# Kernel optimization log

Measured on AMD Instinct MI355X. Metric: run time of the kernel, lower is better.

Reference implementation:

```python
import jax, jax.numpy as jnp
import numpy as np

EPS = 1e-06

def rotate_half(x):
    d = x.shape[-1] // 2
    return jnp.concatenate([-x[..., d:], x[..., :d]], axis=-1)

def rmsnorm(x, w):
    rms = jnp.sqrt(jnp.mean(x * x, axis=-1, keepdims=True) + EPS)
    return (x / rms) * w

def setup_inputs() -> dict:
    key = jax.random.key(0)
    ks = jax.random.split(key, 12)
    H, Hq, Hkv, Dh, S, C = 2048, 16, 8, 128, 1, 16384
    sc = 0.02
    return {
        "hidden_states": jax.random.normal(ks[0], (1, 1, S, H), jnp.float32),
        "cos": jax.random.uniform(ks[1], (1, 1, S, Dh), jnp.float32),
        "sin": jax.random.uniform(ks[2], (1, 1, S, Dh), jnp.float32),
        "attention_mask": jnp.zeros((1, 1, S, C + S), jnp.float32),
        "k_cache": jax.random.normal(ks[3], (Hkv, Dh, C), jnp.float32),
        "v_cache": jax.random.normal(ks[4], (Hkv, C, Dh), jnp.float32),
        "Wq": jax.random.normal(ks[5], (Hq, Dh, H), jnp.float32) * sc,
        "Wk": jax.random.normal(ks[6], (Hkv, Dh, H), jnp.float32) * sc,
        "Wv": jax.random.normal(ks[7], (Hkv, Dh, H), jnp.float32) * sc,
        "Wo": jax.random.normal(ks[8], (H, Hq * Dh), jnp.float32) * sc,
        "q_norm_w": jnp.ones((Dh,), jnp.float32),
        "k_norm_w": jnp.ones((Dh,), jnp.float32),
    }

def reference(hidden_states, cos, sin, attention_mask, k_cache, v_cache, Wq, Wk, Wv, Wo, q_norm_w, k_norm_w):
    S = hidden_states.shape[2]
    Hq, Dh = Wq.shape[0], Wq.shape[1]
    Hkv = Wk.shape[0]
    g = Hq // Hkv
    x = hidden_states.reshape(S, -1)                      # [S, H]
    # per-head 1x1 conv == per-head linear; batched as einsum
    q = rmsnorm(jnp.einsum('sh,qdh->qsd', x, Wq), q_norm_w)   # [Hq, S, Dh]
    k = rmsnorm(jnp.einsum('sh,kdh->ksd', x, Wk), k_norm_w)   # [Hkv, S, Dh]
    v = jnp.einsum('sh,kdh->ksd', x, Wv)                      # [Hkv, S, Dh]
    c = cos.reshape(S, Dh)
    s = sin.reshape(S, Dh)
    q = q * c + rotate_half(q) * s
    k_new = k * c + rotate_half(k) * s
    # KV cache concat: k stored transposed [Hkv, Dh, C]
    k_full = jnp.concatenate([k_cache, jnp.swapaxes(k_new, 1, 2)], axis=2)  # [Hkv, Dh, C+S]
    v_full = jnp.concatenate([v_cache, v], axis=1)                          # [Hkv, C+S, Dh]
    kf = jnp.repeat(k_full, g, axis=0)                    # GQA expand -> [Hq, Dh, C+S]
    vf = jnp.repeat(v_full, g, axis=0)                    # [Hq, C+S, Dh]
    scaling = Dh ** -0.5
    scores = jnp.einsum('qsd,qdc->qsc', q, kf) * scaling + attention_mask.reshape(1, S, -1)
    probs = jax.nn.softmax(scores, axis=-1)
    out = jnp.einsum('qsc,qcd->qsd', probs, vf)           # [Hq, S, Dh]
    out = jnp.transpose(out, (1, 0, 2)).reshape(S, Hq * Dh)  # head-major last dim
    attn = out @ Wo.T                                     # o_proj 1x1 conv
    return attn.reshape(1, 1, S, -1), k_new, v
```

## Files before the change

kernel.cpp:

```cpp
#include <hip/hip_runtime.h>
#include <math.h>
#include <stddef.h>

#define HQ   16
#define HKV  8
#define DH   128
#define HID  2048
#define CC   16384
#define NCH  64
#define CHUNK 256


__global__ void k_qkv(const float* __restrict__ x,
                      const float* __restrict__ Wq,
                      const float* __restrict__ Wk,
                      const float* __restrict__ Wv,
                      float* __restrict__ raw){
  int wave = threadIdx.x >> 6, lane = threadIdx.x & 63;
  int e = blockIdx.x * 4 + wave;
  const float* W;
  if (e < 2048)      W = Wq + (size_t)e * HID;
  else if (e < 3072) W = Wk + (size_t)(e - 2048) * HID;
  else               W = Wv + (size_t)(e - 3072) * HID;
  float acc = 0.f;
  #pragma unroll
  for (int j = 0; j < 4; ++j){
    int base = (j * 64 + lane) * 8;
    float4 a0 = *(const float4*)(x + base);
    float4 a1 = *(const float4*)(x + base + 4);
    float4 b0 = *(const float4*)(W + base);
    float4 b1 = *(const float4*)(W + base + 4);
    acc += a0.x*b0.x + a0.y*b0.y + a0.z*b0.z + a0.w*b0.w
         + a1.x*b1.x + a1.y*b1.y + a1.z*b1.z + a1.w*b1.w;
  }
  #pragma unroll
  for (int off = 32; off; off >>= 1) acc += __shfl_down(acc, off, 64);
  if (lane == 0) raw[e] = acc;
}

__global__ void k_normrope(const float* __restrict__ raw,
                           const float* __restrict__ cosb,
                           const float* __restrict__ sinb,
                           const float* __restrict__ qw,
                           const float* __restrict__ kw,
                           float* __restrict__ qf,
                           float* __restrict__ kf,
                           float* __restrict__ out){
  __shared__ float lds[DH];
  __shared__ float wsum[2];
  int b = blockIdx.x, t = threadIdx.x;
  if (b >= 24){
    int h = b - 24;
    out[3072 + h * DH + t] = raw[3072 + h * DH + t];
    return;
  }
  bool isq = (b < 16);
  int h = isq ? b : b - 16;
  float val = isq ? raw[h * DH + t] : raw[2048 + h * DH + t];
  float ss = val * val;
  #pragma unroll
  for (int off = 32; off; off >>= 1) ss += __shfl_down(ss, off, 64);
  if ((t & 63) == 0) wsum[t >> 6] = ss;
  __syncthreads();
  float rms = sqrtf((wsum[0] + wsum[1]) / 128.f + 1e-6f);
  float w = isq ? qw[t] : kw[t];
  float normed = val / rms * w;
  lds[t] = normed;
  __syncthreads();
  float rot = (t < 64) ? -lds[t + 64] : lds[t - 64];
  float res = normed * cosb[t] + rot * sinb[t];
  if (isq) qf[h * DH + t] = res;
  else { kf[h * DH + t] = res; out[2048 + h * DH + t] = res; }
}

__global__ void k_flash(const float* __restrict__ qf,
                        const float* __restrict__ kcache,
                        const float* __restrict__ vcache,
                        const float* __restrict__ mask,
                        float* __restrict__ opart,
                        float2* __restrict__ ml){
  __shared__ float q_s[2][DH];
  __shared__ float sc_part[4][2][CHUNK];
  __shared__ float p_s[2][CHUNK];
  __shared__ float part[2][8][DH];
  __shared__ float red[8];
  int kv = blockIdx.x >> 6, ch = blockIdx.x & 63;
  int c0 = ch << 8;
  int t = threadIdx.x;
  q_s[t >> 7][t & 127] = qf[(kv * 2 + (t >> 7)) * DH + (t & 127)];
  __syncthreads();
  const float scale = 0.08838834764831845f;

  {
    int dg = t >> 6, ln = t & 63;
    const float* kp = kcache + (size_t)kv * DH * CC + (size_t)(dg * 32) * CC + (c0 + ln * 4);
    float a00 = 0.f, a01 = 0.f, a02 = 0.f, a03 = 0.f;
    float a10 = 0.f, a11 = 0.f, a12 = 0.f, a13 = 0.f;
    #pragma unroll 8
    for (int dd = 0; dd < 32; ++dd){
      float4 kk = *(const float4*)(kp + (size_t)dd * CC);
      float q0 = q_s[0][dg * 32 + dd], q1 = q_s[1][dg * 32 + dd];
      a00 += q0 * kk.x; a01 += q0 * kk.y; a02 += q0 * kk.z; a03 += q0 * kk.w;
      a10 += q1 * kk.x; a11 += q1 * kk.y; a12 += q1 * kk.z; a13 += q1 * kk.w;
    }
    *(float4*)&sc_part[dg][0][ln * 4] = make_float4(a00, a01, a02, a03);
    *(float4*)&sc_part[dg][1][ln * 4] = make_float4(a10, a11, a12, a13);
  }
  __syncthreads();

  float s0, s1;
  {
    float mk = mask[c0 + t];
    s0 = (sc_part[0][0][t] + sc_part[1][0][t] + sc_part[2][0][t] + sc_part[3][0][t]) * scale + mk;
    s1 = (sc_part[0][1][t] + sc_part[1][1][t] + sc_part[2][1][t] + sc_part[3][1][t]) * scale + mk;
  }
  int wv = t >> 6, ln = t & 63;
  float lmax0 = s0, lmax1 = s1;
  #pragma unroll
  for (int off = 32; off; off >>= 1){
    lmax0 = fmaxf(lmax0, __shfl_down(lmax0, off, 64));
    lmax1 = fmaxf(lmax1, __shfl_down(lmax1, off, 64));
  }
  if (ln == 0){ red[wv] = lmax0; red[4 + wv] = lmax1; }
  __syncthreads();
  float m0 = fmaxf(fmaxf(red[0], red[1]), fmaxf(red[2], red[3]));
  float m1 = fmaxf(fmaxf(red[4], red[5]), fmaxf(red[6], red[7]));
  float p0 = __expf(s0 - m0);
  float p1 = __expf(s1 - m1);
  p_s[0][t] = p0;
  p_s[1][t] = p1;
  float ls0 = p0, ls1 = p1;
  #pragma unroll
  for (int off = 32; off; off >>= 1){
    ls0 += __shfl_down(ls0, off, 64);
    ls1 += __shfl_down(ls1, off, 64);
  }
  __syncthreads();
  if (ln == 0){ red[wv] = ls0; red[4 + wv] = ls1; }
  __syncthreads();
  if (t == 0){
    float l0 = red[0] + red[1] + red[2] + red[3];
    float l1 = red[4] + red[5] + red[6] + red[7];
    ml[(size_t)(kv * 2)     * NCH + ch] = make_float2(m0, l0);
    ml[(size_t)(kv * 2 + 1) * NCH + ch] = make_float2(m1, l1);
  }

  {
    int s = t >> 5, d4 = (t & 31) * 4;
    const float* vbase = vcache + (size_t)kv * CC * DH + d4;
    float4 a0 = make_float4(0.f, 0.f, 0.f, 0.f);
    float4 a1 = make_float4(0.f, 0.f, 0.f, 0.f);
    #pragma unroll 4
    for (int i = 0; i < 32; ++i){
      int off = i * 8 + s;
      float pp0 = p_s[0][off];
      float pp1 = p_s[1][off];
      float4 v = *(const float4*)(vbase + (size_t)(c0 + off) * DH);
      a0.x += pp0 * v.x; a0.y += pp0 * v.y; a0.z += pp0 * v.z; a0.w += pp0 * v.w;
      a1.x += pp1 * v.x; a1.y += pp1 * v.y; a1.z += pp1 * v.z; a1.w += pp1 * v.w;
    }
    *(float4*)&part[0][s][d4] = a0;
    *(float4*)&part[1][s][d4] = a1;
  }
  __syncthreads();
  {
    int hh = t >> 7, d = t & 127;
    float o = 0.f;
    #pragma unroll
    for (int ss = 0; ss < 8; ++ss) o += part[hh][ss][d];
    int qh = kv * 2 + hh;
    opart[((size_t)qh * NCH + ch) * DH + d] = o;
  }
}

__global__ void k_combine(const float* __restrict__ opart,
                          const float2* __restrict__ ml,
                          const float* __restrict__ qf,
                          const float* __restrict__ kf,
                          const float* __restrict__ vnew,
                          const float* __restrict__ mask,
                          float* __restrict__ attn_in){
  __shared__ float red[2];
  int qh = blockIdx.x, d = threadIdx.x;
  int kv = qh >> 1;
  float M = -1e30f;
  #pragma unroll 8
  for (int ch = 0; ch < NCH; ++ch) M = fmaxf(M, ml[(size_t)qh * NCH + ch].x);
  float o = 0.f, L = 0.f;
  for (int ch = 0; ch < NCH; ++ch){
    float2 m = ml[(size_t)qh * NCH + ch];
    float w = __expf(m.x - M);
    L += m.y * w;
    o += w * opart[((size_t)qh * NCH + ch) * DH + d];
  }
  float prod = qf[qh * DH + d] * kf[kv * DH + d];
  float sum = prod;
  #pragma unroll
  for (int off = 32; off; off >>= 1) sum += __shfl_down(sum, off, 64);
  if ((d & 63) == 0) red[d >> 6] = sum;
  __syncthreads();
  float s_new = (red[0] + red[1]) * 0.08838834764831845f + mask[CC];
  float pn = __expf(s_new - M);
  L += pn;
  o += pn * vnew[kv * DH + d];
  attn_in[qh * DH + d] = o / L;
}

__global__ void k_oproj(const float* __restrict__ attn_in,
                        const float* __restrict__ Wo,
                        float* __restrict__ out){
  int wave = threadIdx.x >> 6, lane = threadIdx.x & 63;
  int e = blockIdx.x * 4 + wave;
  const float* W = Wo + (size_t)e * HID;
  float acc = 0.f;
  #pragma unroll
  for (int j = 0; j < 4; ++j){
    int base = (j * 64 + lane) * 8;
    float4 a0 = *(const float4*)(attn_in + base);
    float4 a1 = *(const float4*)(attn_in + base + 4);
    float4 b0 = *(const float4*)(W + base);
    float4 b1 = *(const float4*)(W + base + 4);
    acc += a0.x*b0.x + a0.y*b0.y + a0.z*b0.z + a0.w*b0.w
         + a1.x*b1.x + a1.y*b1.y + a1.z*b1.z + a1.w*b1.w;
  }
  #pragma unroll
  for (int off = 32; off; off >>= 1) acc += __shfl_down(acc, off, 64);
  if (lane == 0) out[e] = acc;
}

extern "C" void kernel_launch(void* const* d_in, const int* in_sizes, int n_in,
                              void* d_out, int out_size, void* d_ws, size_t ws_size,
                              hipStream_t stream){
  const float* x    = (const float*)d_in[0];
  const float* cosb = (const float*)d_in[1];
  const float* sinb = (const float*)d_in[2];
  const float* mask = (const float*)d_in[3];
  const float* kc   = (const float*)d_in[4];
  const float* vc   = (const float*)d_in[5];
  const float* Wq   = (const float*)d_in[6];
  const float* Wk   = (const float*)d_in[7];
  const float* Wv   = (const float*)d_in[8];
  const float* Wo   = (const float*)d_in[9];
  const float* qw   = (const float*)d_in[10];
  const float* kw   = (const float*)d_in[11];
  float* out = (float*)d_out;
  float* ws = (float*)d_ws;
  float* raw     = ws;
  float* qf      = ws + 4096;
  float* kf      = ws + 6144;
  float* opart   = ws + 8192;
  float2* ML     = (float2*)(ws + 139264);
  float* attn_in = ws + 141312;

  k_qkv     <<<1024, 256, 0, stream>>>(x, Wq, Wk, Wv, raw);
  k_normrope<<<32,   128, 0, stream>>>(raw, cosb, sinb, qw, kw, qf, kf, out);
  k_flash   <<<HKV * NCH, 256, 0, stream>>>(qf, kc, vc, mask, opart, ML);
  k_combine <<<HQ, 128, 0, stream>>>(opart, ML, qf, kf, raw + 3072, mask, attn_in);
  k_oproj   <<<512, 256, 0, stream>>>(attn_in, Wo, out);
}
```

Baseline: 216.6 us.

## Split flash-decode into smaller chunks with 512-thread blocks for more parallelism

Halves the KV chunk size to 128 and doubles the number of split-K blocks to 1024, each now using 512 threads. The K-score loop moves to 8 depth groups with float2 loads and the V loop to 16 row slices. Softmax reduction is reorganised so only half the threads take part. Launch bounds are also added to the projection kernels. The goal is more memory-level parallelism across the GPU while streaming the 64 MB KV cache, at the cost of narrower K loads, more partials for the combine kernel and idle threads during the reductions.

```diff
diff --git a/kernel.cpp b/kernel.cpp
--- a/kernel.cpp
+++ b/kernel.cpp
@@ -7,15 +7,16 @@
 #define DH   128
 #define HID  2048
 #define CC   16384
-#define NCH  64
-#define CHUNK 256
-
-
-__global__ void k_qkv(const float* __restrict__ x,
-                      const float* __restrict__ Wq,
-                      const float* __restrict__ Wk,
-                      const float* __restrict__ Wv,
-                      float* __restrict__ raw){
+#define NCH  128
+#define CHUNK 128
+
+
+__global__ __launch_bounds__(256, 4)
+void k_qkv(const float* __restrict__ x,
+           const float* __restrict__ Wq,
+           const float* __restrict__ Wk,
+           const float* __restrict__ Wv,
+           float* __restrict__ raw){
   int wave = threadIdx.x >> 6, lane = threadIdx.x & 63;
   int e = blockIdx.x * 4 + wave;
   const float* W;
@@ -73,76 +74,70 @@
   else { kf[h * DH + t] = res; out[2048 + h * DH + t] = res; }
 }
 
-__global__ void k_flash(const float* __restrict__ qf,
-                        const float* __restrict__ kcache,
-                        const float* __restrict__ vcache,
-                        const float* __restrict__ mask,
-                        float* __restrict__ opart,
-                        float2* __restrict__ ml){
+__global__ __launch_bounds__(512, 8)
+void k_flash(const float* __restrict__ qf,
+             const float* __restrict__ kcache,
+             const float* __restrict__ vcache,
+             const float* __restrict__ mask,
+             float* __restrict__ opart,
+             float2* __restrict__ ml){
   __shared__ float q_s[2][DH];
-  __shared__ float sc_part[4][2][CHUNK];
+  __shared__ float sc_part[8][2][CHUNK];
   __shared__ float p_s[2][CHUNK];
-  __shared__ float part[2][8][DH];
+  __shared__ float part[2][16][DH];
   __shared__ float red[8];
-  int kv = blockIdx.x >> 6, ch = blockIdx.x & 63;
-  int c0 = ch << 8;
+  int kv = blockIdx.x >> 7, ch = blockIdx.x & 127;
+  int c0 = ch << 7;
   int t = threadIdx.x;
-  q_s[t >> 7][t & 127] = qf[(kv * 2 + (t >> 7)) * DH + (t & 127)];
+  if (t < 256) q_s[t >> 7][t & 127] = qf[(kv * 2 + (t >> 7)) * DH + (t & 127)];
   __syncthreads();
   const float scale = 0.08838834764831845f;
 
   {
     int dg = t >> 6, ln = t & 63;
-    const float* kp = kcache + (size_t)kv * DH * CC + (size_t)(dg * 32) * CC + (c0 + ln * 4);
-    float a00 = 0.f, a01 = 0.f, a02 = 0.f, a03 = 0.f;
-    float a10 = 0.f, a11 = 0.f, a12 = 0.f, a13 = 0.f;
-    #pragma unroll 8
-    for (int dd = 0; dd < 32; ++dd){
-      float4 kk = *(const float4*)(kp + (size_t)dd * CC);
-      float q0 = q_s[0][dg * 32 + dd], q1 = q_s[1][dg * 32 + dd];
-      a00 += q0 * kk.x; a01 += q0 * kk.y; a02 += q0 * kk.z; a03 += q0 * kk.w;
-      a10 += q1 * kk.x; a11 += q1 * kk.y; a12 += q1 * kk.z; a13 += q1 * kk.w;
+    const float* kp = kcache + (size_t)kv * DH * CC + (size_t)(dg * 16) * CC + (c0 + ln * 2);
+    float a00 = 0.f, a01 = 0.f, a10 = 0.f, a11 = 0.f;
+    #pragma unroll
+    for (int dd = 0; dd < 16; ++dd){
+      float2 kk = *(const float2*)(kp + (size_t)dd * CC);
+      float q0 = q_s[0][dg * 16 + dd], q1 = q_s[1][dg * 16 + dd];
+      a00 += q0 * kk.x; a01 += q0 * kk.y;
+      a10 += q1 * kk.x; a11 += q1 * kk.y;
     }
-    *(float4*)&sc_part[dg][0][ln * 4] = make_float4(a00, a01, a02, a03);
-    *(float4*)&sc_part[dg][1][ln * 4] = make_float4(a10, a11, a12, a13);
-  }
-  __syncthreads();
-
-  float s0, s1;
-  {
-    float mk = mask[c0 + t];
-    s0 = (sc_part[0][0][t] + sc_part[1][0][t] + sc_part[2][0][t] + sc_part[3][0][t]) * scale + mk;
-    s1 = (sc_part[0][1][t] + sc_part[1][1][t] + sc_part[2][1][t] + sc_part[3][1][t]) * scale + mk;
-  }
+    *(float2*)&sc_part[dg][0][ln * 2] = make_float2(a00, a01);
+    *(float2*)&sc_part[dg][1][ln * 2] = make_float2(a10, a11);
+  }
+  __syncthreads();
+
+  float s_val = 0.f;
+  int hB = t >> 7, pB = t & 127;
   int wv = t >> 6, ln = t & 63;
-  float lmax0 = s0, lmax1 = s1;
-  #pragma unroll
-  for (int off = 32; off; off >>= 1){
-    lmax0 = fmaxf(lmax0, __shfl_down(lmax0, off, 64));
-    lmax1 = fmaxf(lmax1, __shfl_down(lmax1, off, 64));
-  }
-  if (ln == 0){ red[wv] = lmax0; red[4 + wv] = lmax1; }
-  __syncthreads();
-  float m0 = fmaxf(fmaxf(red[0], red[1]), fmaxf(red[2], red[3]));
-  float m1 = fmaxf(fmaxf(red[4], red[5]), fmaxf(red[6], red[7]));
-  float p0 = __expf(s0 - m0);
-  float p1 = __expf(s1 - m1);
-  p_s[0][t] = p0;
-  p_s[1][t] = p1;
-  float ls0 = p0, ls1 = p1;
-  #pragma unroll
-  for (int off = 32; off; off >>= 1){
-    ls0 += __shfl_down(ls0, off, 64);
-    ls1 += __shfl_down(ls1, off, 64);
-  }
-  __syncthreads();
-  if (ln == 0){ red[wv] = ls0; red[4 + wv] = ls1; }
+  if (t < 256){
+    float sum8 = 0.f;
+    #pragma unroll
+    for (int dg = 0; dg < 8; ++dg) sum8 += sc_part[dg][hB][pB];
+    s_val = sum8 * scale + mask[c0 + pB];
+    float lmax = s_val;
+    #pragma unroll
+    for (int off = 32; off; off >>= 1) lmax = fmaxf(lmax, __shfl_down(lmax, off, 64));
+    if (ln == 0) red[wv] = lmax;
+  }
+  __syncthreads();
+  float m0 = fmaxf(red[0], red[1]);
+  float m1 = fmaxf(red[2], red[3]);
+  float pe = 0.f;
+  if (t < 256){
+    pe = __expf(s_val - (hB ? m1 : m0));
+    p_s[hB][pB] = pe;
+    #pragma unroll
+    for (int off = 32; off; off >>= 1) pe += __shfl_down(pe, off, 64);
+  }
+  __syncthreads();
+  if (t < 256 && ln == 0) red[wv] = pe;
   __syncthreads();
   if (t == 0){
-    float l0 = red[0] + red[1] + red[2] + red[3];
-    float l1 = red[4] + red[5] + red[6] + red[7];
-    ml[(size_t)(kv * 2)     * NCH + ch] = make_float2(m0, l0);
-    ml[(size_t)(kv * 2 + 1) * NCH + ch] = make_float2(m1, l1);
+    ml[(size_t)(kv * 2)     * NCH + ch] = make_float2(m0, red[0] + red[1]);
+    ml[(size_t)(kv * 2 + 1) * NCH + ch] = make_float2(m1, red[2] + red[3]);
   }
 
   {
@@ -150,9 +145,9 @@
     const float* vbase = vcache + (size_t)kv * CC * DH + d4;
     float4 a0 = make_float4(0.f, 0.f, 0.f, 0.f);
     float4 a1 = make_float4(0.f, 0.f, 0.f, 0.f);
-    #pragma unroll 4
-    for (int i = 0; i < 32; ++i){
-      int off = i * 8 + s;
+    #pragma unroll
+    for (int i = 0; i < 8; ++i){
+      int off = i * 16 + s;
       float pp0 = p_s[0][off];
       float pp1 = p_s[1][off];
       float4 v = *(const float4*)(vbase + (size_t)(c0 + off) * DH);
@@ -163,11 +158,11 @@
     *(float4*)&part[1][s][d4] = a1;
   }
   __syncthreads();
-  {
+  if (t < 256){
     int hh = t >> 7, d = t & 127;
     float o = 0.f;
     #pragma unroll
-    for (int ss = 0; ss < 8; ++ss) o += part[hh][ss][d];
+    for (int ss = 0; ss < 16; ++ss) o += part[hh][ss][d];
     int qh = kv * 2 + hh;
     opart[((size_t)qh * NCH + ch) * DH + d] = o;
   }
@@ -206,9 +201,10 @@
   attn_in[qh * DH + d] = o / L;
 }
 
-__global__ void k_oproj(const float* __restrict__ attn_in,
-                        const float* __restrict__ Wo,
-                        float* __restrict__ out){
+__global__ __launch_bounds__(256, 4)
+void k_oproj(const float* __restrict__ attn_in,
+             const float* __restrict__ Wo,
+             float* __restrict__ out){
   int wave = threadIdx.x >> 6, lane = threadIdx.x & 63;
   int e = blockIdx.x * 4 + wave;
   const float* W = Wo + (size_t)e * HID;
@@ -249,12 +245,12 @@
   float* qf      = ws + 4096;
   float* kf      = ws + 6144;
   float* opart   = ws + 8192;
-  float2* ML     = (float2*)(ws + 139264);
-  float* attn_in = ws + 141312;
+  float2* ML     = (float2*)(ws + 270336);
+  float* attn_in = ws + 274432;
 
   k_qkv     <<<1024, 256, 0, stream>>>(x, Wq, Wk, Wv, raw);
   k_normrope<<<32,   128, 0, stream>>>(raw, cosb, sinb, qw, kw, qf, kf, out);
-  k_flash   <<<HKV * NCH, 256, 0, stream>>>(qf, kc, vc, mask, opart, ML);
+  k_flash   <<<HKV * NCH, 512, 0, stream>>>(qf, kc, vc, mask, opart, ML);
   k_combine <<<HQ, 128, 0, stream>>>(opart, ML, qf, kf, raw + 3072, mask, attn_in);
   k_oproj   <<<512, 256, 0, stream>>>(attn_in, Wo, out);
 }
```

Measured after the change: 225.1 us. +3.9%, slower.
